# Performance work log

Measured on AMD Instinct MI355X. Metric: run time of the kernel, lower is better.

Reference implementation:

```python
import jax, jax.numpy as jnp
import numpy as np

SMOOTHING = 0.1
EPSILON = 1e-08


def setup_inputs() -> dict:
    key = jax.random.key(0)
    k1, k2 = jax.random.split(key)
    B, S, C = 2, 2048, 32000
    outputs = jax.random.normal(k1, (B, S, C), dtype=jnp.float32)
    gold_label_ids = jax.random.randint(k2, (B, S), 0, C, dtype=jnp.int64)
    mask = jnp.ones((B, S), dtype=bool)
    weight = jnp.ones((C,), dtype=jnp.float32)
    return {"outputs": outputs, "gold_label_ids": gold_label_ids, "mask": mask, "weight": weight}


def reference(outputs, gold_label_ids, mask, weight):
    B, S, C = outputs.shape
    N = B * S
    logits = outputs.reshape(N, C)
    gold = gold_label_ids.reshape(N)

    nll = -jax.nn.log_softmax(logits, axis=-1)  # [N, C]

    # Label-smoothed target: uniform = s/(C-1) everywhere, confidence at gold.
    # loss_i = sum_c w_c * nll_ic * smooth_ic
    #        = uniform * sum_c(w_c * nll_ic) + (confidence - uniform) * w_g * nll_ig
    uniform = SMOOTHING / (C - 1)
    confidence = 1.0 - SMOOTHING
    total = jnp.einsum('nc,c->n', nll, weight)  # sum of weighted nll per row
    gold_nll = jnp.take_along_axis(nll, gold[:, None], axis=1)[:, 0]
    gold_w = weight[gold]
    loss = uniform * total + (confidence - uniform) * gold_w * gold_nll  # [N]

    seq_mask = mask.reshape(N).astype(loss.dtype)
    loss = loss * seq_mask
    return jnp.sum(loss) / (jnp.sum(seq_mask) + EPSILON)
```

## Files before the change

### kernel.cpp

```cpp
#include <hip/hip_runtime.h>
#include <math.h>

#define SMOOTHING 0.1f
#define EPSILON_F 1e-8f

__device__ __forceinline__ void osm_combine(float& m, float& s, float mo, float so) {
    float nm = fmaxf(m, mo);
    s = s * __expf(m - nm) + so * __expf(mo - nm);
    m = nm;
}

__device__ __forceinline__ void osm_update4(float& m, float& s, float4 v,
                                            float4 w, float& wd, float& ws) {
    float c01 = fmaxf(v.x, v.y);
    float c23 = fmaxf(v.z, v.w);
    float cm  = fmaxf(c01, c23);
    float nm  = fmaxf(m, cm);
    float e   = __expf(m - nm);
    float e0  = __expf(v.x - nm);
    float e1  = __expf(v.y - nm);
    float e2  = __expf(v.z - nm);
    float e3  = __expf(v.w - nm);
    s = fmaf(s, e, (e0 + e1) + (e2 + e3));
    m = nm;
    wd = fmaf(w.x, v.x, wd);
    wd = fmaf(w.y, v.y, wd);
    wd = fmaf(w.z, v.z, wd);
    wd = fmaf(w.w, v.w, wd);
    ws += (w.x + w.y) + (w.z + w.w);
}

__global__ __launch_bounds__(256) void Seq2SeqLoss_row_kernel(
    const float* __restrict__ logits,
    const int*   __restrict__ gold,
    const int*   __restrict__ mask,
    const float* __restrict__ weight,
    float*       __restrict__ row_loss,
    int C)
{
    const int row = blockIdx.x;
    const int tid = threadIdx.x;
    const float* __restrict__ x = logits + (size_t)row * (size_t)C;

    const int C4   = C >> 2;
    const int half = C4 >> 1;
    const float4* __restrict__ x4 = (const float4*)x;
    const float4* __restrict__ w4 = (const float4*)weight;

    float m0 = -1e30f, s0 = 0.f;
    float m1 = -1e30f, s1 = 0.f;
    float wd = 0.f, wsum = 0.f;

    for (int i = tid; i < half; i += 256) {
        float4 a  = x4[i];
        float4 b  = x4[i + half];
        float4 wa = w4[i];
        float4 wb = w4[i + half];
        osm_update4(m0, s0, a, wa, wd, wsum);
        osm_update4(m1, s1, b, wb, wd, wsum);
    }
    for (int i = (half << 1) + tid; i < C4; i += 256) {
        float4 a  = x4[i];
        float4 wa = w4[i];
        osm_update4(m0, s0, a, wa, wd, wsum);
    }

    osm_combine(m0, s0, m1, s1);
    float M = m0, S = s0;

    #pragma unroll
    for (int off = 32; off >= 1; off >>= 1) {
        float Mo = __shfl_down(M, off);
        float So = __shfl_down(S, off);
        wd   += __shfl_down(wd, off);
        wsum += __shfl_down(wsum, off);
        osm_combine(M, S, Mo, So);
    }

    __shared__ float shM[4], shS[4], shWD[4], shWS[4];
    const int wave = tid >> 6;
    if ((tid & 63) == 0) { shM[wave] = M; shS[wave] = S; shWD[wave] = wd; shWS[wave] = wsum; }
    __syncthreads();

    if (tid == 0) {
        #pragma unroll
        for (int w = 1; w < 4; ++w) {
            osm_combine(M, S, shM[w], shS[w]);
            wd   += shWD[w];
            wsum += shWS[w];
        }
        float logZ = M + logf(S);

        int   g  = gold[row];
        float xg = x[g];
        float wg = weight[g];

        const float uniform    = SMOOTHING / (float)(C - 1);
        const float confidence = 1.0f - SMOOTHING;

        float total    = logZ * wsum - wd;
        float gold_nll = logZ - xg;
        float loss = uniform * total + (confidence - uniform) * wg * gold_nll;

        loss *= (mask[row] != 0) ? 1.0f : 0.0f;
        row_loss[row] = loss;
    }
}

__global__ __launch_bounds__(256) void Seq2SeqLoss_finalize_kernel(
    const float* __restrict__ row_loss,
    const int*   __restrict__ mask,
    float*       __restrict__ out,
    int N)
{
    const int tid = threadIdx.x;
    float acc = 0.f, cnt = 0.f;
    for (int i = tid; i < N; i += 256) {
        acc += row_loss[i];
        cnt += (mask[i] != 0) ? 1.0f : 0.0f;
    }
    #pragma unroll
    for (int off = 32; off >= 1; off >>= 1) {
        acc += __shfl_down(acc, off);
        cnt += __shfl_down(cnt, off);
    }
    __shared__ float shA[4], shC[4];
    const int wave = tid >> 6;
    if ((tid & 63) == 0) { shA[wave] = acc; shC[wave] = cnt; }
    __syncthreads();
    if (tid == 0) {
        #pragma unroll
        for (int w = 1; w < 4; ++w) { acc += shA[w]; cnt += shC[w]; }
        out[0] = acc / (cnt + EPSILON_F);
    }
}

extern "C" void kernel_launch(void* const* d_in, const int* in_sizes, int n_in,
                              void* d_out, int out_size, void* d_ws, size_t ws_size,
                              hipStream_t stream) {
    const float* logits = (const float*)d_in[0];
    const int*   gold   = (const int*)d_in[1];
    const int*   mask   = (const int*)d_in[2];
    const float* weight = (const float*)d_in[3];

    const int N = in_sizes[1];
    const int C = in_sizes[3];

    float* row_loss = (float*)d_ws;

    Seq2SeqLoss_row_kernel<<<N, 256, 0, stream>>>(logits, gold, mask, weight, row_loss, C);
    Seq2SeqLoss_finalize_kernel<<<1, 256, 0, stream>>>(row_loss, mask, (float*)d_out, N);
}
```

Measured before the change: 669.4 us.

## Use deferred-max online softmax with exp2, nontemporal loads, wider finalize

Rewrites the online log-sum-exp update so the running max is only rescaled when a new value exceeds it by a threshold, which drops the per-step rescale exponential and uses hardware exp2 with a precomputed scaled offset. Logit loads become nontemporal, the gold, mask and weight lookups are hoisted to the start of the kernel, and the finalize kernel uses 1024 threads. The aim is to cut transcendental and ALU work so the row kernel is bound by memory bandwidth. The threshold allows the sum to hold values up to about e^10 before rescaling, which is safe in fp32 but adds a data-dependent branch.

```diff
diff --git a/kernel.cpp b/kernel.cpp
--- a/kernel.cpp
+++ b/kernel.cpp
@@ -3,26 +3,38 @@
 
 #define SMOOTHING 0.1f
 #define EPSILON_F 1e-8f
+#define LOG2E_F   1.44269504088896340736f
+#define DEFER_THR 10.0f
+
+typedef float vf4 __attribute__((ext_vector_type(4)));
+
+__device__ __forceinline__ float fexp2(float x) { return __builtin_amdgcn_exp2f(x); }
+
+__device__ __forceinline__ vf4 ntload4(const vf4* p) {
+    return __builtin_nontemporal_load(p);
+}
 
 __device__ __forceinline__ void osm_combine(float& m, float& s, float mo, float so) {
     float nm = fmaxf(m, mo);
-    s = s * __expf(m - nm) + so * __expf(mo - nm);
+    s = s * fexp2((m - nm) * LOG2E_F) + so * fexp2((mo - nm) * LOG2E_F);
     m = nm;
 }
 
-__device__ __forceinline__ void osm_update4(float& m, float& s, float4 v,
-                                            float4 w, float& wd, float& ws) {
+__device__ __forceinline__ void osm_update4(float& M, float& nMs, float& S,
+                                            vf4 v, vf4 w, float& wd, float& ws) {
     float c01 = fmaxf(v.x, v.y);
     float c23 = fmaxf(v.z, v.w);
     float cm  = fmaxf(c01, c23);
-    float nm  = fmaxf(m, cm);
-    float e   = __expf(m - nm);
-    float e0  = __expf(v.x - nm);
-    float e1  = __expf(v.y - nm);
-    float e2  = __expf(v.z - nm);
-    float e3  = __expf(v.w - nm);
-    s = fmaf(s, e, (e0 + e1) + (e2 + e3));
-    m = nm;
+    if (__builtin_expect(cm > M + DEFER_THR, 0)) {
+        S *= fexp2((M - cm) * LOG2E_F);
+        M = cm;
+        nMs = -M * LOG2E_F;
+    }
+    float e0 = fexp2(fmaf(v.x, LOG2E_F, nMs));
+    float e1 = fexp2(fmaf(v.y, LOG2E_F, nMs));
+    float e2 = fexp2(fmaf(v.z, LOG2E_F, nMs));
+    float e3 = fexp2(fmaf(v.w, LOG2E_F, nMs));
+    S += (e0 + e1) + (e2 + e3);
     wd = fmaf(w.x, v.x, wd);
     wd = fmaf(w.y, v.y, wd);
     wd = fmaf(w.z, v.z, wd);
@@ -42,31 +54,38 @@
     const int tid = threadIdx.x;
     const float* __restrict__ x = logits + (size_t)row * (size_t)C;
 
+    const int   g  = gold[row];
+    const int   mk = mask[row];
+    const float xg = x[g];
+    const float wg = weight[g];
+
     const int C4   = C >> 2;
     const int half = C4 >> 1;
-    const float4* __restrict__ x4 = (const float4*)x;
-    const float4* __restrict__ w4 = (const float4*)weight;
+    const vf4* __restrict__ x4  = (const vf4*)x;
+    const vf4* __restrict__ x4h = x4 + half;
+    const vf4* __restrict__ w4  = (const vf4*)weight;
+    const vf4* __restrict__ w4h = w4 + half;
 
-    float m0 = -1e30f, s0 = 0.f;
-    float m1 = -1e30f, s1 = 0.f;
+    float M0 = -1e30f, nMs0 = 0.f, S0 = 0.f;
+    float M1 = -1e30f, nMs1 = 0.f, S1 = 0.f;
     float wd = 0.f, wsum = 0.f;
 
     for (int i = tid; i < half; i += 256) {
-        float4 a  = x4[i];
-        float4 b  = x4[i + half];
-        float4 wa = w4[i];
-        float4 wb = w4[i + half];
-        osm_update4(m0, s0, a, wa, wd, wsum);
-        osm_update4(m1, s1, b, wb, wd, wsum);
+        vf4 a  = ntload4(x4  + i);
+        vf4 b  = ntload4(x4h + i);
+        vf4 wa = w4[i];
+        vf4 wb = w4h[i];
+        osm_update4(M0, nMs0, S0, a, wa, wd, wsum);
+        osm_update4(M1, nMs1, S1, b, wb, wd, wsum);
     }
     for (int i = (half << 1) + tid; i < C4; i += 256) {
-        float4 a  = x4[i];
-        float4 wa = w4[i];
-        osm_update4(m0, s0, a, wa, wd, wsum);
+        vf4 a  = ntload4(x4 + i);
+        vf4 wa = w4[i];
+        osm_update4(M0, nMs0, S0, a, wa, wd, wsum);
     }
 
-    osm_combine(m0, s0, m1, s1);
-    float M = m0, S = s0;
+    osm_combine(M0, S0, M1, S1);
+    float M = M0, S = S0;
 
     #pragma unroll
     for (int off = 32; off >= 1; off >>= 1) {
@@ -91,10 +110,6 @@
         }
         float logZ = M + logf(S);
 
-        int   g  = gold[row];
-        float xg = x[g];
-        float wg = weight[g];
-
         const float uniform    = SMOOTHING / (float)(C - 1);
         const float confidence = 1.0f - SMOOTHING;
 
@@ -102,12 +117,12 @@
         float gold_nll = logZ - xg;
         float loss = uniform * total + (confidence - uniform) * wg * gold_nll;
 
-        loss *= (mask[row] != 0) ? 1.0f : 0.0f;
+        loss *= (mk != 0) ? 1.0f : 0.0f;
         row_loss[row] = loss;
     }
 }
 
-__global__ __launch_bounds__(256) void Seq2SeqLoss_finalize_kernel(
+__global__ __launch_bounds__(1024) void Seq2SeqLoss_finalize_kernel(
     const float* __restrict__ row_loss,
     const int*   __restrict__ mask,
     float*       __restrict__ out,
@@ -115,7 +130,7 @@
 {
     const int tid = threadIdx.x;
     float acc = 0.f, cnt = 0.f;
-    for (int i = tid; i < N; i += 256) {
+    for (int i = tid; i < N; i += 1024) {
         acc += row_loss[i];
         cnt += (mask[i] != 0) ? 1.0f : 0.0f;
     }
@@ -124,13 +139,13 @@
         acc += __shfl_down(acc, off);
         cnt += __shfl_down(cnt, off);
     }
-    __shared__ float shA[4], shC[4];
+    __shared__ float shA[16], shC[16];
     const int wave = tid >> 6;
     if ((tid & 63) == 0) { shA[wave] = acc; shC[wave] = cnt; }
     __syncthreads();
     if (tid == 0) {
         #pragma unroll
-        for (int w = 1; w < 4; ++w) { acc += shA[w]; cnt += shC[w]; }
+        for (int w = 1; w < 16; ++w) { acc += shA[w]; cnt += shC[w]; }
         out[0] = acc / (cnt + EPSILON_F);
     }
 }
@@ -149,5 +164,5 @@
     float* row_loss = (float*)d_ws;
 
     Seq2SeqLoss_row_kernel<<<N, 256, 0, stream>>>(logits, gold, mask, weight, row_loss, C);
-    Seq2SeqLoss_finalize_kernel<<<1, 256, 0, stream>>>(row_loss, mask, (float*)d_out, N);
+    Seq2SeqLoss_finalize_kernel<<<1, 1024, 0, stream>>>(row_loss, mask, (float*)d_out, N);
 }
```

After: 643.5 us. 1.04x faster.
